# Kernel optimization log

Hardware: AMD Instinct MI355X
Metric: run time of the kernel (lower is better)

Reference implementation:

```python
import jax, jax.numpy as jnp
import numpy as np

B, I, O, S, C = 64, 2048, 2048, 10, 512  # batch, input, output, dendritic segments, context dim


def setup_inputs() -> dict:
    key = jax.random.key(0)
    ks = jax.random.split(key, 8)
    x = jax.random.normal(ks[0], (B, I), dtype=jnp.float32)
    context = jax.random.normal(ks[1], (B, C), dtype=jnp.float32)
    prev_activation = jax.random.normal(ks[2], (B, I), dtype=jnp.float32)
    # sparse-initialized weight: randn/sqrt(I) * (rand > sparsity)
    w = jax.random.normal(ks[3], (O, I), dtype=jnp.float32) / np.sqrt(I)
    mask = (jax.random.uniform(ks[4], (O, I)) > 0.9).astype(jnp.float32)
    weight = w * mask
    bias = jnp.zeros((O,), dtype=jnp.float32)
    astrocyte_activation = jnp.ones((O,), dtype=jnp.float32)
    astrocyte_threshold = jnp.full((O,), 0.5, dtype=jnp.float32)
    dendrite_segments = jax.random.normal(ks[5], (O, I, S), dtype=jnp.float32) / np.sqrt(I)
    dendritic_gates = jnp.ones((O, S), dtype=jnp.float32)
    connection_strength = jnp.ones((O, I), dtype=jnp.float32)
    pruning_threshold = jnp.full((1,), 0.01, dtype=jnp.float32)
    return {
        "x": x, "context": context, "prev_activation": prev_activation,
        "weight": weight, "bias": bias,
        "astrocyte_activation": astrocyte_activation,
        "astrocyte_threshold": astrocyte_threshold,
        "dendrite_segments": dendrite_segments,
        "dendritic_gates": dendritic_gates,
        "connection_strength": connection_strength,
        "pruning_threshold": pruning_threshold,
    }


def reference(x, context, prev_activation, weight, bias, astrocyte_activation,
              astrocyte_threshold, dendrite_segments, dendritic_gates,
              connection_strength, pruning_threshold):
    dt = x.dtype
    # structural plasticity (eval branch): prune weak connections
    conn_mask = (jnp.abs(weight) * connection_strength > pruning_threshold[0]).astype(dt)
    eff_w = weight * conn_mask  # [O, I]
    # astrocyte modulation
    ctx_signal = jnp.mean(context, axis=-1, keepdims=True)          # [B, 1]
    astro = jax.nn.sigmoid(ctx_signal * astrocyte_activation[None, :])  # [B, O]
    astro = astro * (astro > astrocyte_threshold[None, :]).astype(dt)
    mean_astro = jnp.mean(astro, axis=0)                            # [O]
    mod_w = eff_w * mean_astro[:, None]                             # [O, I]
    synaptic = x @ mod_w.T + bias                                   # [B, O]
    # multi-compartment dendritic processing
    seg_act = jnp.einsum('bi,ois->bos', x, dendrite_segments)       # [B, O, S]
    gated = jax.nn.relu(seg_act) * jax.nn.sigmoid(dendritic_gates)[None, :, :]
    dendritic = jnp.sum(gated, axis=-1)                             # [B, O]
    return jax.nn.relu(synaptic + dendritic)
```

## Files before the change

### kernel.cpp

```cpp
#include <hip/hip_runtime.h>
#include <math.h>

#define Bn 64
#define In 2048
#define On 2048
#define Sn 10
#define Cn 512

#define OT 4
#define KT 64
#define NP 48
#define LROW 72
#define NSTAGE (In / KT)

typedef short short8 __attribute__((ext_vector_type(8)));
typedef float f32x4 __attribute__((ext_vector_type(4)));
typedef unsigned short ushort4v __attribute__((ext_vector_type(4)));

__device__ __forceinline__ unsigned short f2bf(float f) {
    union { float f; unsigned u; } v; v.f = f;
    unsigned r = (v.u + 0x7FFFu + ((v.u >> 16) & 1u)) >> 16;
    return (unsigned short)r;
}

__global__ void prep_kernel(const float* __restrict__ x,
                            const float* __restrict__ ctx,
                            float* __restrict__ ws_ctx,
                            unsigned short* __restrict__ ws_xbf) {
    const int b = blockIdx.x;
    const int t = threadIdx.x;
    if (b < Bn) {
        __shared__ float red[256];
        float s = ctx[b * Cn + t] + ctx[b * Cn + t + 256];
        red[t] = s;
        __syncthreads();
        for (int off = 128; off > 0; off >>= 1) {
            if (t < off) red[t] += red[t + off];
            __syncthreads();
        }
        if (t == 0) ws_ctx[b] = red[0] * (1.0f / (float)Cn);
    } else {
        int idx = (b - Bn) * 256 + t;
        ws_xbf[idx] = f2bf(x[idx]);
    }
}

__global__ __launch_bounds__(256, 2)
void main_kernel(const unsigned short* __restrict__ xbf,
                 const float* __restrict__ wgt,
                 const float* __restrict__ cst,
                 const float* __restrict__ seg,
                 const float* __restrict__ bias,
                 const float* __restrict__ aact,
                 const float* __restrict__ athr,
                 const float* __restrict__ gates,
                 const float* __restrict__ prn,
                 const float* __restrict__ ws_ctx,
                 float* __restrict__ out) {
    __shared__ __align__(16) unsigned short Alds[2][64 * LROW];
    __shared__ __align__(16) unsigned short Blds[2][NP * LROW];
    __shared__ float dsum[Bn][OT];
    __shared__ float ssum[Bn][OT];
    __shared__ float mastro[OT];

    const int t = threadIdx.x;
    const int o0 = blockIdx.x * OT;
    const int wave = t >> 6;
    const int lane = t & 63;
    const int l15 = lane & 15;
    const int q = lane >> 4;
    const float pthr = prn[0];

    ((float*)dsum)[t] = 0.0f;
    ((float*)ssum)[t] = 0.0f;

    for (int idx = t; idx < 4 * LROW; idx += 256) {
        Blds[0][44 * LROW + idx] = 0;
        Blds[1][44 * LROW + idx] = 0;
    }

    if (t < OT) {
        const int o = o0 + t;
        const float aa = aact[o], th = athr[o];
        float sum = 0.0f;
        for (int b2 = 0; b2 < Bn; ++b2) {
            float sg = 1.0f / (1.0f + expf(-ws_ctx[b2] * aa));
            if (sg > th) sum += sg;
        }
        mastro[t] = sum * (1.0f / (float)Bn);
    }

    const int s_o = t >> 6;
    const int s_i = t & 63;
    const float* segp = seg + ((size_t)(o0 + s_o) * In + s_i) * Sn;
    const int xm0 = t >> 3;
    const int xk0 = (t & 7) * 8;
    const int xm1 = 32 + (t >> 3);
    const int w_o = t >> 4;
    const int w_k = (t & 15) * 4;

    float sreg[10];
    short8 xv0, xv1;
    f32x4 wv, cv;

    auto load_stage = [&](int i0) {
        const float* sp = segp + (size_t)i0 * Sn;
#pragma unroll
        for (int r2 = 0; r2 < 5; ++r2) {
            float2 tmp = *(const float2*)(sp + r2 * 2);
            sreg[2 * r2] = tmp.x;
            sreg[2 * r2 + 1] = tmp.y;
        }
        xv0 = *(const short8*)(xbf + xm0 * In + i0 + xk0);
        xv1 = *(const short8*)(xbf + xm1 * In + i0 + xk0);
        if (t < 64) {
            wv = *(const f32x4*)(wgt + (size_t)(o0 + w_o) * In + i0 + w_k);
            cv = *(const f32x4*)(cst + (size_t)(o0 + w_o) * In + i0 + w_k);
        }
    };

    auto store_stage = [&](int bb) {
        unsigned short* Bp = &Blds[bb][(s_o * 10) * LROW + s_i];
#pragma unroll
        for (int s = 0; s < 10; ++s) Bp[s * LROW] = f2bf(sreg[s]);
        *(short8*)&Alds[bb][xm0 * LROW + xk0] = xv0;
        *(short8*)&Alds[bb][xm1 * LROW + xk0] = xv1;
        if (t < 64) {
            unsigned short ev[4];
#pragma unroll
            for (int j = 0; j < 4; ++j) {
                float wj = wv[j];
                float e = (__builtin_fabsf(wj) * cv[j] > pthr) ? wj : 0.0f;
                ev[j] = f2bf(e);
            }
            ushort4v e4 = {ev[0], ev[1], ev[2], ev[3]};
            *(ushort4v*)&Blds[bb][(40 + w_o) * LROW + w_k] = e4;
        }
    };

    f32x4 acc[3];
#pragma unroll
    for (int n = 0; n < 3; ++n) acc[n] = (f32x4){0.f, 0.f, 0.f, 0.f};

    auto compute = [&](int bb) {
        const unsigned short* Ap = &Alds[bb][(wave * 16 + l15) * LROW + q * 8];
        const unsigned short* Bp = &Blds[bb][l15 * LROW + q * 8];
#pragma unroll
        for (int ks = 0; ks < KT; ks += 32) {
            short8 a  = *(const short8*)(Ap + ks);
            short8 b0 = *(const short8*)(Bp + ks);
            short8 b1 = *(const short8*)(Bp + 16 * LROW + ks);
            short8 b2 = *(const short8*)(Bp + 32 * LROW + ks);
            acc[0] = __builtin_amdgcn_mfma_f32_16x16x32_bf16(a, b0, acc[0], 0, 0, 0);
            acc[1] = __builtin_amdgcn_mfma_f32_16x16x32_bf16(a, b1, acc[1], 0, 0, 0);
            acc[2] = __builtin_amdgcn_mfma_f32_16x16x32_bf16(a, b2, acc[2], 0, 0, 0);
        }
    };

    load_stage(0);
    store_stage(0);
    __syncthreads();
    int bb = 0;
    for (int it = 1; it < NSTAGE; ++it) {
        load_stage(it * KT);
        compute(bb);
        store_stage(bb ^ 1);
        __syncthreads();
        bb ^= 1;
    }
    compute(bb);

    const int brow = wave * 16 + q * 4;
#pragma unroll
    for (int nt = 0; nt < 3; ++nt) {
        const int n = nt * 16 + l15;
        if (n < 40) {
            const int ol = n / 10;
            const int s = n - ol * 10;
            const float g = 1.0f / (1.0f + expf(-gates[(o0 + ol) * Sn + s]));
#pragma unroll
            for (int r = 0; r < 4; ++r) {
                float v = acc[nt][r];
                v = v > 0.0f ? v : 0.0f;
                atomicAdd(&dsum[brow + r][ol], v * g);
            }
        } else if (n < 44) {
            const int ol = n - 40;
#pragma unroll
            for (int r = 0; r < 4; ++r) ssum[brow + r][ol] = acc[nt][r];
        }
    }
    __syncthreads();
    {
        const int m = t >> 2;
        const int ol = t & 3;
        const int o = o0 + ol;
        float v = dsum[m][ol] + mastro[ol] * ssum[m][ol] + bias[o];
        out[(size_t)m * On + o] = v > 0.0f ? v : 0.0f;
    }
}

extern "C" void kernel_launch(void* const* d_in, const int* in_sizes, int n_in,
                              void* d_out, int out_size, void* d_ws, size_t ws_size,
                              hipStream_t stream) {
    (void)in_sizes; (void)n_in; (void)out_size; (void)ws_size;
    const float* x    = (const float*)d_in[0];
    const float* ctx  = (const float*)d_in[1];
    const float* wgt  = (const float*)d_in[3];
    const float* bias = (const float*)d_in[4];
    const float* aact = (const float*)d_in[5];
    const float* athr = (const float*)d_in[6];
    const float* seg  = (const float*)d_in[7];
    const float* gat  = (const float*)d_in[8];
    const float* cst  = (const float*)d_in[9];
    const float* prn  = (const float*)d_in[10];
    float* out = (float*)d_out;

    float* ws_ctx = (float*)d_ws;
    unsigned short* ws_xbf = (unsigned short*)((char*)d_ws + 256);

    prep_kernel<<<Bn + (Bn * In) / 256, 256, 0, stream>>>(x, ctx, ws_ctx, ws_xbf);
    main_kernel<<<On / OT, 256, 0, stream>>>(ws_xbf, wgt, cst, seg, bias, aact,
                                             athr, gat, prn, ws_ctx, out);
}
```

Before: 291.3 us.

## Split K across blocks with partial-sum workspace and separate finalize kernel

The main GEMM kernel now splits the input dimension into four ranges, so four times as many blocks run, each writing per-segment partial sums to a workspace. A new finalize kernel reduces the partials and applies ReLU, gate sigmoid, the astrocyte scale and bias. Astrocyte means move to their own small kernel. Segment loads are reorganized to be coalesced across lanes, x is read directly from global memory instead of LDS, and occupancy is raised to 8 blocks per SM. This costs a single-buffered LDS stage, extra partial-sum traffic (about 25 MB written and read back) and two extra launches.

```diff
diff --git a/kernel.cpp b/kernel.cpp
--- a/kernel.cpp
+++ b/kernel.cpp
@@ -8,10 +8,12 @@
 #define Cn 512
 
 #define OT 4
-#define KT 64
-#define NP 48
-#define LROW 72
-#define NSTAGE (In / KT)
+#define KSPLIT 4
+#define KRANGE (In / KSPLIT)
+#define KT 128
+#define NSTG (KRANGE / KT)
+#define LROW 136
+#define SLOT 12
 
 typedef short short8 __attribute__((ext_vector_type(8)));
 typedef float f32x4 __attribute__((ext_vector_type(4)));
@@ -31,8 +33,7 @@
     const int t = threadIdx.x;
     if (b < Bn) {
         __shared__ float red[256];
-        float s = ctx[b * Cn + t] + ctx[b * Cn + t + 256];
-        red[t] = s;
+        red[t] = ctx[b * Cn + t] + ctx[b * Cn + t + 256];
         __syncthreads();
         for (int off = 128; off > 0; off >>= 1) {
             if (t < off) red[t] += red[t + off];
@@ -45,159 +46,151 @@
     }
 }
 
-__global__ __launch_bounds__(256, 2)
+__global__ void mastro_kernel(const float* __restrict__ aact,
+                              const float* __restrict__ athr,
+                              const float* __restrict__ ws_ctx,
+                              float* __restrict__ ws_mastro) {
+    const int o = blockIdx.x * 256 + threadIdx.x;
+    const float aa = aact[o], th = athr[o];
+    float sum = 0.0f;
+    for (int b = 0; b < Bn; ++b) {
+        float sg = 1.0f / (1.0f + expf(-ws_ctx[b] * aa));
+        if (sg > th) sum += sg;
+    }
+    ws_mastro[o] = sum * (1.0f / (float)Bn);
+}
+
+__global__ __launch_bounds__(256, 8)
 void main_kernel(const unsigned short* __restrict__ xbf,
                  const float* __restrict__ wgt,
                  const float* __restrict__ cst,
                  const float* __restrict__ seg,
-                 const float* __restrict__ bias,
-                 const float* __restrict__ aact,
-                 const float* __restrict__ athr,
-                 const float* __restrict__ gates,
                  const float* __restrict__ prn,
-                 const float* __restrict__ ws_ctx,
-                 float* __restrict__ out) {
-    __shared__ __align__(16) unsigned short Alds[2][64 * LROW];
-    __shared__ __align__(16) unsigned short Blds[2][NP * LROW];
-    __shared__ float dsum[Bn][OT];
-    __shared__ float ssum[Bn][OT];
-    __shared__ float mastro[OT];
+                 float* __restrict__ P) {
+    __shared__ __align__(16) unsigned short Blds[48 * LROW];
 
     const int t = threadIdx.x;
-    const int o0 = blockIdx.x * OT;
-    const int wave = t >> 6;
-    const int lane = t & 63;
-    const int l15 = lane & 15;
-    const int q = lane >> 4;
+    const int grp = blockIdx.x >> 2;
+    const int ks  = blockIdx.x & 3;
+    const int o0 = grp * OT;
+    const int ib = ks * KRANGE;
+    const int w = t >> 6, l = t & 63;
+    const int l15 = l & 15, q = l >> 4;
     const float pthr = prn[0];
 
-    ((float*)dsum)[t] = 0.0f;
-    ((float*)ssum)[t] = 0.0f;
-
-    for (int idx = t; idx < 4 * LROW; idx += 256) {
-        Blds[0][44 * LROW + idx] = 0;
-        Blds[1][44 * LROW + idx] = 0;
-    }
-
-    if (t < OT) {
-        const int o = o0 + t;
-        const float aa = aact[o], th = athr[o];
-        float sum = 0.0f;
-        for (int b2 = 0; b2 < Bn; ++b2) {
-            float sg = 1.0f / (1.0f + expf(-ws_ctx[b2] * aa));
-            if (sg > th) sum += sg;
-        }
-        mastro[t] = sum * (1.0f / (float)Bn);
-    }
-
-    const int s_o = t >> 6;
-    const int s_i = t & 63;
-    const float* segp = seg + ((size_t)(o0 + s_o) * In + s_i) * Sn;
-    const int xm0 = t >> 3;
-    const int xk0 = (t & 7) * 8;
-    const int xm1 = 32 + (t >> 3);
-    const int w_o = t >> 4;
-    const int w_k = (t & 15) * 4;
-
-    float sreg[10];
-    short8 xv0, xv1;
-    f32x4 wv, cv;
-
-    auto load_stage = [&](int i0) {
-        const float* sp = segp + (size_t)i0 * Sn;
-#pragma unroll
-        for (int r2 = 0; r2 < 5; ++r2) {
-            float2 tmp = *(const float2*)(sp + r2 * 2);
-            sreg[2 * r2] = tmp.x;
-            sreg[2 * r2 + 1] = tmp.y;
-        }
-        xv0 = *(const short8*)(xbf + xm0 * In + i0 + xk0);
-        xv1 = *(const short8*)(xbf + xm1 * In + i0 + xk0);
-        if (t < 64) {
-            wv = *(const f32x4*)(wgt + (size_t)(o0 + w_o) * In + i0 + w_k);
-            cv = *(const f32x4*)(cst + (size_t)(o0 + w_o) * In + i0 + w_k);
-        }
-    };
-
-    auto store_stage = [&](int bb) {
-        unsigned short* Bp = &Blds[bb][(s_o * 10) * LROW + s_i];
-#pragma unroll
-        for (int s = 0; s < 10; ++s) Bp[s * LROW] = f2bf(sreg[s]);
-        *(short8*)&Alds[bb][xm0 * LROW + xk0] = xv0;
-        *(short8*)&Alds[bb][xm1 * LROW + xk0] = xv1;
-        if (t < 64) {
-            unsigned short ev[4];
-#pragma unroll
-            for (int j = 0; j < 4; ++j) {
-                float wj = wv[j];
-                float e = (__builtin_fabsf(wj) * cv[j] > pthr) ? wj : 0.0f;
-                ev[j] = f2bf(e);
-            }
-            ushort4v e4 = {ev[0], ev[1], ev[2], ev[3]};
-            *(ushort4v*)&Blds[bb][(40 + w_o) * LROW + w_k] = e4;
-        }
-    };
+    for (int idx = t; idx < 4 * LROW; idx += 256) Blds[44 * LROW + idx] = 0;
 
     f32x4 acc[3];
 #pragma unroll
     for (int n = 0; n < 3; ++n) acc[n] = (f32x4){0.f, 0.f, 0.f, 0.f};
 
-    auto compute = [&](int bb) {
-        const unsigned short* Ap = &Alds[bb][(wave * 16 + l15) * LROW + q * 8];
-        const unsigned short* Bp = &Blds[bb][l15 * LROW + q * 8];
-#pragma unroll
-        for (int ks = 0; ks < KT; ks += 32) {
-            short8 a  = *(const short8*)(Ap + ks);
-            short8 b0 = *(const short8*)(Bp + ks);
-            short8 b1 = *(const short8*)(Bp + 16 * LROW + ks);
-            short8 b2 = *(const short8*)(Bp + 32 * LROW + ks);
+    const float* segw = seg + ((size_t)(o0 + w) * In) * Sn;
+
+    for (int is = 0; is < NSTG; ++is) {
+        const int i0 = ib + is * KT;
+
+        unsigned psv[10];
+        {
+            const float* sp = segw + (size_t)i0 * Sn;
+#pragma unroll
+            for (int c = 0; c < 10; ++c) {
+                float2 f2 = *(const float2*)(sp + c * 128 + 2 * l);
+                psv[c] = (unsigned)f2bf(f2.x) | ((unsigned)f2bf(f2.y) << 16);
+            }
+        }
+        ushort4v ew[2];
+        if (w == 0) {
+#pragma unroll
+            for (int i = 0; i < 2; ++i) {
+                const int o_l = i * 2 + (l >> 5);
+                const int col = (l & 31) * 4;
+                f32x4 wv = *(const f32x4*)(wgt + (size_t)(o0 + o_l) * In + i0 + col);
+                f32x4 cv = *(const f32x4*)(cst + (size_t)(o0 + o_l) * In + i0 + col);
+#pragma unroll
+                for (int j = 0; j < 4; ++j) {
+                    float wj = wv[j];
+                    ew[i][j] = f2bf((__builtin_fabsf(wj) * cv[j] > pthr) ? wj : 0.0f);
+                }
+            }
+        }
+
+        __syncthreads();
+
+#pragma unroll
+        for (int c = 0; c < 10; ++c) {
+            unsigned j = (unsigned)(c * 128 + 2 * l);
+            unsigned ii = j / 10u;
+            unsigned s = j - ii * 10u;
+            unsigned short* bp = &Blds[(w * Sn + s) * LROW + ii];
+            bp[0] = (unsigned short)psv[c];
+            bp[LROW] = (unsigned short)(psv[c] >> 16);
+        }
+        if (w == 0) {
+#pragma unroll
+            for (int i = 0; i < 2; ++i) {
+                const int o_l = i * 2 + (l >> 5);
+                const int col = (l & 31) * 4;
+                *(ushort4v*)&Blds[(40 + o_l) * LROW + col] = ew[i];
+            }
+        }
+        __syncthreads();
+
+        const unsigned short* xrow = xbf + (size_t)(w * 16 + l15) * In + i0 + q * 8;
+#pragma unroll
+        for (int kk = 0; kk < KT; kk += 32) {
+            short8 a  = *(const short8*)(xrow + kk);
+            short8 b0 = *(const short8*)&Blds[(0  + l15) * LROW + q * 8 + kk];
+            short8 b1 = *(const short8*)&Blds[(16 + l15) * LROW + q * 8 + kk];
+            short8 b2 = *(const short8*)&Blds[(32 + l15) * LROW + q * 8 + kk];
             acc[0] = __builtin_amdgcn_mfma_f32_16x16x32_bf16(a, b0, acc[0], 0, 0, 0);
             acc[1] = __builtin_amdgcn_mfma_f32_16x16x32_bf16(a, b1, acc[1], 0, 0, 0);
             acc[2] = __builtin_amdgcn_mfma_f32_16x16x32_bf16(a, b2, acc[2], 0, 0, 0);
         }
-    };
-
-    load_stage(0);
-    store_stage(0);
-    __syncthreads();
-    int bb = 0;
-    for (int it = 1; it < NSTAGE; ++it) {
-        load_stage(it * KT);
-        compute(bb);
-        store_stage(bb ^ 1);
-        __syncthreads();
-        bb ^= 1;
-    }
-    compute(bb);
-
-    const int brow = wave * 16 + q * 4;
+    }
+
 #pragma unroll
     for (int nt = 0; nt < 3; ++nt) {
-        const int n = nt * 16 + l15;
-        if (n < 40) {
-            const int ol = n / 10;
-            const int s = n - ol * 10;
-            const float g = 1.0f / (1.0f + expf(-gates[(o0 + ol) * Sn + s]));
-#pragma unroll
-            for (int r = 0; r < 4; ++r) {
-                float v = acc[nt][r];
-                v = v > 0.0f ? v : 0.0f;
-                atomicAdd(&dsum[brow + r][ol], v * g);
-            }
-        } else if (n < 44) {
-            const int ol = n - 40;
-#pragma unroll
-            for (int r = 0; r < 4; ++r) ssum[brow + r][ol] = acc[nt][r];
-        }
-    }
-    __syncthreads();
-    {
-        const int m = t >> 2;
-        const int ol = t & 3;
-        const int o = o0 + ol;
-        float v = dsum[m][ol] + mastro[ol] * ssum[m][ol] + bias[o];
-        out[(size_t)m * On + o] = v > 0.0f ? v : 0.0f;
-    }
+        const unsigned n = nt * 16 + l15;
+#pragma unroll
+        for (int r = 0; r < 4; ++r) {
+            const int m = w * 16 + q * 4 + r;
+            const size_t base = (((size_t)ks * Bn + m) * On + o0) * SLOT;
+            if (n < 40u) {
+                unsigned ol = n / 10u, s = n - ol * 10u;
+                P[base + ol * SLOT + s] = acc[nt][r];
+            } else if (n < 44u) {
+                P[base + (n - 40u) * SLOT + 10] = acc[nt][r];
+            }
+        }
+    }
+}
+
+__global__ void finalize_kernel(const float* __restrict__ P,
+                                const float* __restrict__ gates,
+                                const float* __restrict__ bias,
+                                const float* __restrict__ ws_mastro,
+                                float* __restrict__ out) {
+    const int t = threadIdx.x;
+    const int o = (blockIdx.x & 31) * 64 + (t & 63);
+    const int b = (blockIdx.x >> 5) * 4 + (t >> 6);
+    f32x4 v0 = {0.f, 0.f, 0.f, 0.f}, v1 = v0, v2 = v0;
+#pragma unroll
+    for (int ks = 0; ks < KSPLIT; ++ks) {
+        const f32x4* p = (const f32x4*)(P + (((size_t)ks * Bn + b) * On + o) * SLOT);
+        v0 += p[0]; v1 += p[1]; v2 += p[2];
+    }
+    float d[12];
+#pragma unroll
+    for (int j = 0; j < 4; ++j) { d[j] = v0[j]; d[4 + j] = v1[j]; d[8 + j] = v2[j]; }
+    float dend = 0.0f;
+#pragma unroll
+    for (int s = 0; s < Sn; ++s) {
+        float g = 1.0f / (1.0f + expf(-gates[o * Sn + s]));
+        float r = d[s] > 0.0f ? d[s] : 0.0f;
+        dend += r * g;
+    }
+    float val = d[10] * ws_mastro[o] + bias[o] + dend;
+    out[(size_t)b * On + o] = val > 0.0f ? val : 0.0f;
 }
 
 extern "C" void kernel_launch(void* const* d_in, const int* in_sizes, int n_in,
@@ -218,8 +211,11 @@
 
     float* ws_ctx = (float*)d_ws;
     unsigned short* ws_xbf = (unsigned short*)((char*)d_ws + 256);
+    float* ws_mastro = (float*)((char*)d_ws + 262400);
+    float* ws_P = (float*)((char*)d_ws + 270592);
 
     prep_kernel<<<Bn + (Bn * In) / 256, 256, 0, stream>>>(x, ctx, ws_ctx, ws_xbf);
-    main_kernel<<<On / OT, 256, 0, stream>>>(ws_xbf, wgt, cst, seg, bias, aact,
-                                             athr, gat, prn, ws_ctx, out);
-}
+    mastro_kernel<<<On / 256, 256, 0, stream>>>(aact, athr, ws_ctx, ws_mastro);
+    main_kernel<<<(On / OT) * KSPLIT, 256, 0, stream>>>(ws_xbf, wgt, cst, seg, prn, ws_P);
+    finalize_kernel<<<(On / 64) * (Bn / 4), 256, 0, stream>>>(ws_P, gat, bias, ws_mastro, out);
+}
```

After: 312.2 us. 7.2% more time.
